# Performance work log

Hardware: AMD Instinct MI355X
Metric: run time of the kernel (lower is better)

## Reference

```python
import jax, jax.numpy as jnp
import numpy as np

U = 64  # LSTM_UNITS

def _lstm(xt, kernel, rec, bias):
    # xt: [B, T, 4U]; keras LSTM gate order i, f, g(c), o
    B = xt.shape[0]
    h0 = jnp.zeros((B, U), xt.dtype)
    c0 = jnp.zeros((B, U), xt.dtype)
    def step(carry, x):
        h, c = carry
        z = x @ kernel + h @ rec + bias  # [B, 4U]
        i, f, g, o = jnp.split(z, 4, axis=-1)
        i = jax.nn.sigmoid(i); f = jax.nn.sigmoid(f)
        g = jnp.tanh(g); o = jax.nn.sigmoid(o)
        c = f * c + i * g
        h = o * jnp.tanh(c)
        return (h, c), h
    _, hs = jax.lax.scan(step, (h0, c0), jnp.swapaxes(xt, 0, 1))
    return jnp.swapaxes(hs, 0, 1)  # [B, T, U]

def setup_inputs() -> dict:
    key = jax.random.key(0)
    ks = jax.random.split(key, 12)
    B, T, P = 8, 100, 1000
    pro_id = jax.random.randint(ks[0], (B, T), 0, P, dtype=jnp.int32)
    label = jax.random.randint(ks[1], (B, T), 0, 2, dtype=jnp.int32)
    X = jax.random.normal(ks[2], (P, 2 * U), jnp.float32)
    cos_X = jax.random.uniform(ks[3], (P, P), jnp.float32)
    trimatrix = jnp.tril(jnp.ones((T, T), jnp.float32))  # causal mask [s, t]
    onehot_table = jax.random.normal(ks[4], (2, 4 * U), jnp.float32)
    s = 0.05
    lstm_kernel = jax.random.normal(ks[5], (4 * U, 4 * U), jnp.float32) * s
    lstm_rec = jax.random.normal(ks[6], (U, 4 * U), jnp.float32) * s
    lstm_bias = jnp.zeros((4 * U,), jnp.float32)
    W1 = jax.random.normal(ks[7], (3 * U, 50), jnp.float32) * s
    b1 = jnp.zeros((50,), jnp.float32)
    W2 = jax.random.normal(ks[8], (50, 1), jnp.float32) * s
    b2 = jnp.zeros((1,), jnp.float32)
    return {"pro_id": pro_id, "label": label, "num_pro": P, "X": X,
            "cos_X": cos_X, "trimatrix": trimatrix, "onehot_table": onehot_table,
            "lstm_kernel": lstm_kernel, "lstm_rec": lstm_rec, "lstm_bias": lstm_bias,
            "W1": W1, "b1": b1, "W2": W2, "b2": b2}

def reference(pro_id, label, num_pro, X, cos_X, trimatrix, onehot_table,
              lstm_kernel, lstm_rec, lstm_bias, W1, b1, W2, b2):
    B, T = pro_id.shape
    # one_hot @ X  ==  gather rows of X
    t_X = jnp.tile(X[pro_id], (1, 1, 2))           # [B, T, 4U]
    label_emb = onehot_table[label]                 # [B, T, 4U]
    xt = t_X * label_emb
    ht = _lstm(xt, lstm_kernel, lstm_rec, lstm_bias)  # [B, T, U]
    a = cos_X[pro_id]                               # [B, T, P] (one_hot @ cos_X)
    # ajhj[b,t,p,u] = sum_s tri[s,t] * a[b,s,p] * ht[b,s,u]  (causal weighted sum)
    ajhj = jnp.einsum('bsp,bsu,st->btpu', a, ht, trimatrix)
    XX = jnp.broadcast_to(X[None, None], (B, T, num_pro, 2 * U))
    hatt = jnp.concatenate([ajhj, XX], axis=-1)     # [B, T, P, 3U]
    r = jax.nn.relu(hatt @ W1 + b1)                 # [B, T, P, 50]
    prediction = r @ W2 + b2                        # [B, T, P, 1]
    return prediction
```

## Files before the change

kernel.cpp:

```cpp
#include <hip/hip_runtime.h>
#include <math.h>

#define BB 8
#define TT 100
#define PP 1000
#define NJ 52
#define GROW 56
#define HSTRIDE 68


#define WAVE_BARRIER() asm volatile("s_waitcnt lgkmcnt(0)\ns_barrier" ::: "memory")

__global__ __launch_bounds__(256) void k1_xk(const int* __restrict__ pro_id,
    const int* __restrict__ label, const float* __restrict__ X,
    const float* __restrict__ onehot, const float* __restrict__ kern,
    const float* __restrict__ bias, float* __restrict__ xk)
{
    __shared__ __align__(16) float xt[2][256];
    const int j = threadIdx.x;
    const int r0 = blockIdx.x * 2;
#pragma unroll
    for (int r = 0; r < 2; ++r) {
        int pid = pro_id[r0 + r];
        int lab = label[r0 + r];
        xt[r][j] = X[pid * 128 + (j & 127)] * onehot[lab * 256 + j];
    }
    __syncthreads();
    float acc0 = bias[j], acc1 = acc0;
    float kc[8];
#pragma unroll
    for (int i = 0; i < 8; ++i) kc[i] = kern[i * 256 + j];
    for (int kg = 0; kg < 32; ++kg) {
        float kn[8];
        const int kgn = (kg < 31) ? kg + 1 : 31;
#pragma unroll
        for (int i = 0; i < 8; ++i) kn[i] = kern[(kgn * 8 + i) * 256 + j];
        const int k0 = kg * 8;
        float4 xa0 = *(const float4*)&xt[0][k0];
        float4 xa1 = *(const float4*)&xt[0][k0 + 4];
        float4 xb0 = *(const float4*)&xt[1][k0];
        float4 xb1 = *(const float4*)&xt[1][k0 + 4];
        acc0 += xa0.x * kc[0] + xa0.y * kc[1] + xa0.z * kc[2] + xa0.w * kc[3]
              + xa1.x * kc[4] + xa1.y * kc[5] + xa1.z * kc[6] + xa1.w * kc[7];
        acc1 += xb0.x * kc[0] + xb0.y * kc[1] + xb0.z * kc[2] + xb0.w * kc[3]
              + xb1.x * kc[4] + xb1.y * kc[5] + xb1.z * kc[6] + xb1.w * kc[7];
#pragma unroll
        for (int i = 0; i < 8; ++i) kc[i] = kn[i];
    }
    xk[(r0 + 0) * 256 + j] = acc0;
    xk[(r0 + 1) * 256 + j] = acc1;
}

__global__ __launch_bounds__(256, 1) void mid(const float* __restrict__ xk,
    const float* __restrict__ rec, const float* __restrict__ W1,
    const float* __restrict__ X, const float* __restrict__ b1,
    float* __restrict__ G, float* __restrict__ XcT)
{
    __shared__ __align__(16) float smem[14720];
    const int tid = threadIdx.x;

    if (blockIdx.x < 8) {
        float* h_all = smem;
        float* w1s   = smem + (TT + 1) * HSTRIDE;
        const int b = blockIdx.x;
        const int l = tid & 63;
        const int w = tid >> 6;
        const int u = (w << 4) | (l & 15);
        const int g = l >> 4;
        const int col = (g << 6) | u;

        for (int idx = tid; idx < 3200; idx += 256) {
            int u2 = idx / 50, jj = idx - u2 * 50;
            w1s[u2 * 52 + jj] = W1[idx];
        }
        float rcol[64];
#pragma unroll
        for (int u2 = 0; u2 < 64; ++u2) rcol[u2] = rec[u2 * 256 + col];

        if (tid < 64) h_all[tid] = 0.f;
        float c = 0.f;
        const float* xkb = xk + b * TT * 256;
        float zc0 = xkb[col];
        float zc1 = xkb[256 + col];
        float zc2 = xkb[512 + col];
        __syncthreads();

        for (int t = 0; t < TT; ++t) {
            float a0 = zc0, a1 = 0.f, a2 = 0.f, a3 = 0.f;
            zc0 = zc1; zc1 = zc2;
            int tn = (t + 3 < TT) ? t + 3 : TT - 1;
            zc2 = xkb[tn * 256 + col];
            const float4* h4p = (const float4*)&h_all[t * HSTRIDE];
#pragma unroll
            for (int m = 0; m < 16; ++m) {
                float4 hv = h4p[m];
                a0 += hv.x * rcol[4 * m + 0];
                a1 += hv.y * rcol[4 * m + 1];
                a2 += hv.z * rcol[4 * m + 2];
                a3 += hv.w * rcol[4 * m + 3];
            }
            float z = (a0 + a1) + (a2 + a3);
            float act;
            if (g == 2) act = 2.f / (1.f + __expf(-2.f * z)) - 1.f;
            else        act = 1.f / (1.f + __expf(-z));
            const int base = l & 15;
            float gi = __shfl(act, base);
            float gf = __shfl(act, base + 16);
            float gg = __shfl(act, base + 32);
            float go = __shfl(act, base + 48);
            c = gf * c + gi * gg;
            float h = go * (2.f / (1.f + __expf(-2.f * c)) - 1.f);
            if (g == 0) h_all[(t + 1) * HSTRIDE + u] = h;
            WAVE_BARRIER();
        }
        __syncthreads();

        const int brow0 = b * TT;
        for (int idx = tid; idx < TT * 13; idx += 256) {
            int row = idx / 13;
            int m = idx - row * 13;
            int j = 4 * m;
            const float* hrow = &h_all[(row + 1) * HSTRIDE];
            float ax = 0.f, ay = 0.f, az = 0.f, aw = 0.f;
#pragma unroll
            for (int u4 = 0; u4 < 16; ++u4) {
                float4 hv  = *(const float4*)&hrow[4 * u4];
                float4 w0  = *(const float4*)&w1s[(4 * u4 + 0) * 52 + j];
                float4 w1v = *(const float4*)&w1s[(4 * u4 + 1) * 52 + j];
                float4 w2  = *(const float4*)&w1s[(4 * u4 + 2) * 52 + j];
                float4 w3  = *(const float4*)&w1s[(4 * u4 + 3) * 52 + j];
                ax += hv.x * w0.x + hv.y * w1v.x + hv.z * w2.x + hv.w * w3.x;
                ay += hv.x * w0.y + hv.y * w1v.y + hv.z * w2.y + hv.w * w3.y;
                az += hv.x * w0.z + hv.y * w1v.z + hv.z * w2.z + hv.w * w3.z;
                aw += hv.x * w0.w + hv.y * w1v.w + hv.z * w2.w + hv.w * w3.w;
            }
            if (m == 12) { az = 0.f; aw = 0.f; }
            *(float4*)&G[(brow0 + row) * GROW + j] = make_float4(ax, ay, az, aw);
        }
    } else {
        float* Xs  = smem;
        float* W1T = smem + 8320;
        const int p0 = (blockIdx.x - 8) * 64;
        for (int idx = tid; idx < 6400; idx += 256) {
            int k = idx & 127, jj = idx >> 7;
            W1T[jj * 128 + k] = W1[(64 + k) * 50 + jj];
        }
#pragma unroll
        for (int r = 0; r < 8; ++r) {
            int flat = (tid + 256 * r) * 4;
            int i = flat >> 7;
            int k = flat & 127;
            int p = p0 + i;
            float4 v = make_float4(0.f, 0.f, 0.f, 0.f);
            if (p < PP) v = *(const float4*)&X[p * 128 + k];
            Xs[(k + 0) * 65 + i] = v.x;
            Xs[(k + 1) * 65 + i] = v.y;
            Xs[(k + 2) * 65 + i] = v.z;
            Xs[(k + 3) * 65 + i] = v.w;
        }
        __syncthreads();
        const int ploc = tid & 63;
        const int j0 = tid >> 6;
        float acc[13];
#pragma unroll
        for (int m = 0; m < 13; ++m) {
            int jj = j0 * 13 + m;
            acc[m] = (jj < 50) ? b1[jj] : 0.f;
        }
        for (int k4 = 0; k4 < 32; ++k4) {
            const int k = 4 * k4;
            float x0 = Xs[(k + 0) * 65 + ploc];
            float x1 = Xs[(k + 1) * 65 + ploc];
            float x2 = Xs[(k + 2) * 65 + ploc];
            float x3 = Xs[(k + 3) * 65 + ploc];
#pragma unroll
            for (int m = 0; m < 13; ++m) {
                int jj = j0 * 13 + m;
                if (jj < 50) {
                    float4 wv = *(const float4*)&W1T[jj * 128 + k];
                    acc[m] += x0 * wv.x + x1 * wv.y + x2 * wv.z + x3 * wv.w;
                }
            }
        }
        int p = p0 + ploc;
        if (p < PP) {
#pragma unroll
            for (int m = 0; m < 13; ++m) {
                int jj = j0 * 13 + m;
                if (jj < 50) XcT[jj * PP + p] = acc[m];
            }
        }
        for (int idx = tid; idx < 6 * 64; idx += 256) {
            int r = 50 + (idx >> 6);
            int pp = p0 + (idx & 63);
            if (pp < PP) XcT[r * PP + pp] = 0.f;
        }
    }
}

__global__ __launch_bounds__(256) void k4_main(const int* __restrict__ pro_id,
    const float* __restrict__ cos_X, const float* __restrict__ XcT,
    const float* __restrict__ G, const float* __restrict__ W2,
    const float* __restrict__ b2, float* __restrict__ out)
{
    __shared__ __align__(16) float Gs[TT * GROW];
    __shared__ float w2s[NJ];
    __shared__ int spid[TT];
    const int b = blockIdx.z;
    const int p = blockIdx.y * 256 + threadIdx.x;
    const int ci = blockIdx.x;
    const int t0 = ci * 7;
    const int t1 = (t0 + 7 < TT) ? (t0 + 7) : TT;
    const bool valid = p < PP;
    const int pc = valid ? p : 0;
    const int tid = threadIdx.x;

    {
        const float4* Gg = (const float4*)(G + b * TT * GROW);
        float4* Gd = (float4*)Gs;
        for (int idx = tid; idx < TT * GROW / 4; idx += 256) Gd[idx] = Gg[idx];
        if (tid < TT) spid[tid] = pro_id[b * TT + tid];
        if (tid < NJ) w2s[tid] = (tid < 50) ? W2[tid] : 0.f;
    }

    float V[NJ];
#pragma unroll
    for (int jj = 0; jj < NJ; ++jj) V[jj] = XcT[jj * PP + pc];
    const float b2v = b2[0];
    __syncthreads();

    const float* cb = cos_X + pc;
    float a0 = cb[spid[99] * PP];
    float a1 = cb[spid[98] * PP];
    float a2 = cb[spid[97] * PP];
    float a3 = cb[spid[96] * PP];

    for (int s = TT - 1; s >= t0; --s) {
        float a = a0; a0 = a1; a1 = a2; a2 = a3;
        int sp = s - 4;
        if (sp < t0) sp = t0;
        a3 = cb[spid[sp] * PP];
        const float4* G4 = (const float4*)&Gs[s * GROW];
#pragma unroll
        for (int jv = 0; jv < 13; ++jv) {
            float4 gv = G4[jv];
            V[4 * jv + 0] += a * gv.x;
            V[4 * jv + 1] += a * gv.y;
            V[4 * jv + 2] += a * gv.z;
            V[4 * jv + 3] += a * gv.w;
        }
        if (s < t1) {
            float acc = b2v;
#pragma unroll
            for (int jv = 0; jv < 13; ++jv) {
                float4 wv = *(const float4*)&w2s[4 * jv];
                acc += wv.x * fmaxf(V[4 * jv + 0], 0.f)
                     + wv.y * fmaxf(V[4 * jv + 1], 0.f)
                     + wv.z * fmaxf(V[4 * jv + 2], 0.f)
                     + wv.w * fmaxf(V[4 * jv + 3], 0.f);
            }
            if (valid) out[(b * TT + s) * PP + p] = acc;
        }
    }
}

extern "C" void kernel_launch(void* const* d_in, const int* in_sizes, int n_in,
                              void* d_out, int out_size, void* d_ws, size_t ws_size,
                              hipStream_t stream)
{
    const int* pro_id  = (const int*)d_in[0];
    const int* label   = (const int*)d_in[1];
    const float* X     = (const float*)d_in[3];
    const float* cos_X = (const float*)d_in[4];
    const float* onehot = (const float*)d_in[6];
    const float* lk    = (const float*)d_in[7];
    const float* lr    = (const float*)d_in[8];
    const float* lb    = (const float*)d_in[9];
    const float* W1    = (const float*)d_in[10];
    const float* b1    = (const float*)d_in[11];
    const float* W2    = (const float*)d_in[12];
    const float* b2    = (const float*)d_in[13];

    float* ws  = (float*)d_ws;
    float* xk  = ws;
    float* XcT = ws + 204800;
    float* G   = ws + 260800;
    float* out = (float*)d_out;

    hipLaunchKernelGGL(k1_xk,  dim3(400),      dim3(256), 0, stream,
                       pro_id, label, X, onehot, lk, lb, xk);
    hipLaunchKernelGGL(mid,    dim3(24),       dim3(256), 0, stream,
                       xk, lr, W1, X, b1, G, XcT);
    hipLaunchKernelGGL(k4_main,dim3(15, 4, 8), dim3(256), 0, stream,
                       pro_id, cos_X, XcT, G, W2, b2, out);
}
```

Baseline: 208.4 us.

## Interleave two LSTM batch sequences per block to hide recurrent step latency

The LSTM recurrence now runs two independent batch sequences in each block, 4 blocks instead of 8, interleaving their per-step matvec, activations and shuffles. This is meant to fill the latency bubbles of the serial dependency chain with independent work while sharing the recurrent weights held in registers. The first step is peeled because h0 is zero, and the h buffers drop their padded stride. The cost is more registers and more work per block, and only 4 blocks run the serial section, so the per-step critical path may get longer.

```diff
diff --git a/kernel.cpp b/kernel.cpp
--- a/kernel.cpp
+++ b/kernel.cpp
@@ -6,7 +6,6 @@
 #define PP 1000
 #define NJ 52
 #define GROW 56
-#define HSTRIDE 68
 
 
 #define WAVE_BARRIER() asm volatile("s_waitcnt lgkmcnt(0)\ns_barrier" ::: "memory")
@@ -56,18 +55,20 @@
     const float* __restrict__ X, const float* __restrict__ b1,
     float* __restrict__ G, float* __restrict__ XcT)
 {
-    __shared__ __align__(16) float smem[14720];
+    __shared__ __align__(16) float smem[16128];
     const int tid = threadIdx.x;
 
-    if (blockIdx.x < 8) {
-        float* h_all = smem;
-        float* w1s   = smem + (TT + 1) * HSTRIDE;
+    if (blockIdx.x < 4) {
+        float* hA  = smem;
+        float* hB  = smem + 6400;
+        float* w1s = smem + 12800;
         const int b = blockIdx.x;
         const int l = tid & 63;
         const int w = tid >> 6;
         const int u = (w << 4) | (l & 15);
         const int g = l >> 4;
         const int col = (g << 6) | u;
+        const int base = l & 15;
 
         for (int idx = tid; idx < 3200; idx += 256) {
             int u2 = idx / 50, jj = idx - u2 * 50;
@@ -77,70 +78,102 @@
 #pragma unroll
         for (int u2 = 0; u2 < 64; ++u2) rcol[u2] = rec[u2 * 256 + col];
 
-        if (tid < 64) h_all[tid] = 0.f;
-        float c = 0.f;
-        const float* xkb = xk + b * TT * 256;
-        float zc0 = xkb[col];
-        float zc1 = xkb[256 + col];
-        float zc2 = xkb[512 + col];
+        const float* xkA = xk + b * TT * 256;
+        const float* xkB = xk + (b + 4) * TT * 256;
+        float zA0 = xkA[col], zA1 = xkA[256 + col], zA2 = xkA[512 + col];
+        float zB0 = xkB[col], zB1 = xkB[256 + col], zB2 = xkB[512 + col];
+        float cA = 0.f, cB = 0.f;
+
+        {
+            float zA = zA0, zB = zB0;
+            zA0 = zA1; zA1 = zA2; zA2 = xkA[3 * 256 + col];
+            zB0 = zB1; zB1 = zB2; zB2 = xkB[3 * 256 + col];
+            float actA, actB;
+            if (g == 2) { actA = 2.f / (1.f + __expf(-2.f * zA)) - 1.f;
+                          actB = 2.f / (1.f + __expf(-2.f * zB)) - 1.f; }
+            else        { actA = 1.f / (1.f + __expf(-zA));
+                          actB = 1.f / (1.f + __expf(-zB)); }
+            float giA = __shfl(actA, base),      giB = __shfl(actB, base);
+            float gfA = __shfl(actA, base + 16), gfB = __shfl(actB, base + 16);
+            float ggA = __shfl(actA, base + 32), ggB = __shfl(actB, base + 32);
+            float goA = __shfl(actA, base + 48), goB = __shfl(actB, base + 48);
+            cA = gfA * cA + giA * ggA;
+            cB = gfB * cB + giB * ggB;
+            float hAv = goA * (2.f / (1.f + __expf(-2.f * cA)) - 1.f);
+            float hBv = goB * (2.f / (1.f + __expf(-2.f * cB)) - 1.f);
+            if (g == 0) { hA[u] = hAv; hB[u] = hBv; }
+            WAVE_BARRIER();
+        }
+
+        for (int t = 1; t < TT; ++t) {
+            float aA0 = zA0, aA1 = 0.f, aA2 = 0.f, aA3 = 0.f;
+            float aB0 = zB0, aB1 = 0.f, aB2 = 0.f, aB3 = 0.f;
+            zA0 = zA1; zA1 = zA2;
+            zB0 = zB1; zB1 = zB2;
+            int tn = (t + 3 < TT) ? t + 3 : TT - 1;
+            zA2 = xkA[tn * 256 + col];
+            zB2 = xkB[tn * 256 + col];
+            const float4* hApt = (const float4*)&hA[(t - 1) * 64];
+            const float4* hBpt = (const float4*)&hB[(t - 1) * 64];
+#pragma unroll
+            for (int m = 0; m < 16; ++m) {
+                float4 ha = hApt[m];
+                float4 hb = hBpt[m];
+                aA0 += ha.x * rcol[4 * m + 0]; aB0 += hb.x * rcol[4 * m + 0];
+                aA1 += ha.y * rcol[4 * m + 1]; aB1 += hb.y * rcol[4 * m + 1];
+                aA2 += ha.z * rcol[4 * m + 2]; aB2 += hb.z * rcol[4 * m + 2];
+                aA3 += ha.w * rcol[4 * m + 3]; aB3 += hb.w * rcol[4 * m + 3];
+            }
+            float zA = (aA0 + aA1) + (aA2 + aA3);
+            float zB = (aB0 + aB1) + (aB2 + aB3);
+            float actA, actB;
+            if (g == 2) { actA = 2.f / (1.f + __expf(-2.f * zA)) - 1.f;
+                          actB = 2.f / (1.f + __expf(-2.f * zB)) - 1.f; }
+            else        { actA = 1.f / (1.f + __expf(-zA));
+                          actB = 1.f / (1.f + __expf(-zB)); }
+            float giA = __shfl(actA, base),      giB = __shfl(actB, base);
+            float gfA = __shfl(actA, base + 16), gfB = __shfl(actB, base + 16);
+            float ggA = __shfl(actA, base + 32), ggB = __shfl(actB, base + 32);
+            float goA = __shfl(actA, base + 48), goB = __shfl(actB, base + 48);
+            cA = gfA * cA + giA * ggA;
+            cB = gfB * cB + giB * ggB;
+            float hAv = goA * (2.f / (1.f + __expf(-2.f * cA)) - 1.f);
+            float hBv = goB * (2.f / (1.f + __expf(-2.f * cB)) - 1.f);
+            if (g == 0) { hA[t * 64 + u] = hAv; hB[t * 64 + u] = hBv; }
+            WAVE_BARRIER();
+        }
         __syncthreads();
 
-        for (int t = 0; t < TT; ++t) {
-            float a0 = zc0, a1 = 0.f, a2 = 0.f, a3 = 0.f;
-            zc0 = zc1; zc1 = zc2;
-            int tn = (t + 3 < TT) ? t + 3 : TT - 1;
-            zc2 = xkb[tn * 256 + col];
-            const float4* h4p = (const float4*)&h_all[t * HSTRIDE];
-#pragma unroll
-            for (int m = 0; m < 16; ++m) {
-                float4 hv = h4p[m];
-                a0 += hv.x * rcol[4 * m + 0];
-                a1 += hv.y * rcol[4 * m + 1];
-                a2 += hv.z * rcol[4 * m + 2];
-                a3 += hv.w * rcol[4 * m + 3];
-            }
-            float z = (a0 + a1) + (a2 + a3);
-            float act;
-            if (g == 2) act = 2.f / (1.f + __expf(-2.f * z)) - 1.f;
-            else        act = 1.f / (1.f + __expf(-z));
-            const int base = l & 15;
-            float gi = __shfl(act, base);
-            float gf = __shfl(act, base + 16);
-            float gg = __shfl(act, base + 32);
-            float go = __shfl(act, base + 48);
-            c = gf * c + gi * gg;
-            float h = go * (2.f / (1.f + __expf(-2.f * c)) - 1.f);
-            if (g == 0) h_all[(t + 1) * HSTRIDE + u] = h;
-            WAVE_BARRIER();
-        }
-        __syncthreads();
-
-        const int brow0 = b * TT;
-        for (int idx = tid; idx < TT * 13; idx += 256) {
-            int row = idx / 13;
-            int m = idx - row * 13;
-            int j = 4 * m;
-            const float* hrow = &h_all[(row + 1) * HSTRIDE];
-            float ax = 0.f, ay = 0.f, az = 0.f, aw = 0.f;
-#pragma unroll
-            for (int u4 = 0; u4 < 16; ++u4) {
-                float4 hv  = *(const float4*)&hrow[4 * u4];
-                float4 w0  = *(const float4*)&w1s[(4 * u4 + 0) * 52 + j];
-                float4 w1v = *(const float4*)&w1s[(4 * u4 + 1) * 52 + j];
-                float4 w2  = *(const float4*)&w1s[(4 * u4 + 2) * 52 + j];
-                float4 w3  = *(const float4*)&w1s[(4 * u4 + 3) * 52 + j];
-                ax += hv.x * w0.x + hv.y * w1v.x + hv.z * w2.x + hv.w * w3.x;
-                ay += hv.x * w0.y + hv.y * w1v.y + hv.z * w2.y + hv.w * w3.y;
-                az += hv.x * w0.z + hv.y * w1v.z + hv.z * w2.z + hv.w * w3.z;
-                aw += hv.x * w0.w + hv.y * w1v.w + hv.z * w2.w + hv.w * w3.w;
-            }
-            if (m == 12) { az = 0.f; aw = 0.f; }
-            *(float4*)&G[(brow0 + row) * GROW + j] = make_float4(ax, ay, az, aw);
+#pragma unroll
+        for (int bb2 = 0; bb2 < 2; ++bb2) {
+            const float* hbuf = bb2 ? hB : hA;
+            const int brow0 = (b + 4 * bb2) * TT;
+            for (int idx = tid; idx < TT * 13; idx += 256) {
+                int row = idx / 13;
+                int m = idx - row * 13;
+                int j = 4 * m;
+                const float* hrow = &hbuf[row * 64];
+                float ax = 0.f, ay = 0.f, az = 0.f, aw = 0.f;
+#pragma unroll
+                for (int u4 = 0; u4 < 16; ++u4) {
+                    float4 hv  = *(const float4*)&hrow[4 * u4];
+                    float4 w0  = *(const float4*)&w1s[(4 * u4 + 0) * 52 + j];
+                    float4 w1v = *(const float4*)&w1s[(4 * u4 + 1) * 52 + j];
+                    float4 w2  = *(const float4*)&w1s[(4 * u4 + 2) * 52 + j];
+                    float4 w3  = *(const float4*)&w1s[(4 * u4 + 3) * 52 + j];
+                    ax += hv.x * w0.x + hv.y * w1v.x + hv.z * w2.x + hv.w * w3.x;
+                    ay += hv.x * w0.y + hv.y * w1v.y + hv.z * w2.y + hv.w * w3.y;
+                    az += hv.x * w0.z + hv.y * w1v.z + hv.z * w2.z + hv.w * w3.z;
+                    aw += hv.x * w0.w + hv.y * w1v.w + hv.z * w2.w + hv.w * w3.w;
+                }
+                if (m == 12) { az = 0.f; aw = 0.f; }
+                *(float4*)&G[(brow0 + row) * GROW + j] = make_float4(ax, ay, az, aw);
+            }
         }
     } else {
         float* Xs  = smem;
         float* W1T = smem + 8320;
-        const int p0 = (blockIdx.x - 8) * 64;
+        const int p0 = (blockIdx.x - 4) * 64;
         for (int idx = tid; idx < 6400; idx += 256) {
             int k = idx & 127, jj = idx >> 7;
             W1T[jj * 128 + k] = W1[(64 + k) * 50 + jj];
@@ -289,7 +322,7 @@
 
     hipLaunchKernelGGL(k1_xk,  dim3(400),      dim3(256), 0, stream,
                        pro_id, label, X, onehot, lk, lb, xk);
-    hipLaunchKernelGGL(mid,    dim3(24),       dim3(256), 0, stream,
+    hipLaunchKernelGGL(mid,    dim3(20),       dim3(256), 0, stream,
                        xk, lr, W1, X, b1, G, XcT);
     hipLaunchKernelGGL(k4_main,dim3(15, 4, 8), dim3(256), 0, stream,
                        pro_id, cos_X, XcT, G, W2, b2, out);
```

Result: slower. 242.7 us (+16.5%).
